# Performance work log

Hardware: AMD Instinct MI355X
Metric: run time of the kernel (lower is better)

Reference implementation:

```python
import jax, jax.numpy as jnp
import numpy as np

B, C, D, O = 64, 64, 512, 256
N_REG, G = 8, 8  # 8 regions of 8 channels


def setup_inputs() -> dict:
    key = jax.random.key(0)
    ks = jax.random.split(key, 9)
    std = 0.02  # init_weights_classify: normal(0, 0.02) for Linear weights, zero bias
    x = jax.random.normal(ks[0], (B, C, D), dtype=jnp.float32)
    region_indices = jnp.arange(C, dtype=jnp.int32).reshape(N_REG, G)
    # attn_fc: Linear(2D -> D), ReLU, Linear(D -> 1)
    W1 = jax.random.normal(ks[1], (2 * D, D), dtype=jnp.float32) * std
    b1 = jnp.zeros((D,), jnp.float32)
    W2 = jax.random.normal(ks[2], (D, 1), dtype=jnp.float32) * std
    b2 = jnp.zeros((1,), jnp.float32)
    # gcn1: Linear(D -> D); gcn2: Linear(D -> O)
    Wg1 = jax.random.normal(ks[3], (D, D), dtype=jnp.float32) * std
    bg1 = jnp.zeros((D,), jnp.float32)
    Wg2 = jax.random.normal(ks[4], (D, O), dtype=jnp.float32) * std
    bg2 = jnp.zeros((O,), jnp.float32)
    return {"x": x, "W1": W1, "b1": b1, "W2": W2, "b2": b2,
            "Wg1": Wg1, "bg1": bg1, "Wg2": Wg2, "bg2": bg2,
            "region_indices": region_indices}


def _leaky_relu02(z):
    return jnp.where(z >= 0, z, 0.2 * z)


def reference(x, W1, b1, W2, b2, Wg1, bg1, Wg2, bg2, region_indices):
    Bb, Cc, Dd = x.shape
    n_reg, g = region_indices.shape
    # channel -> region id; mask[i,j] = same region and i != j
    rid = jnp.zeros((Cc,), jnp.int32).at[region_indices.reshape(-1)].set(
        jnp.repeat(jnp.arange(n_reg, dtype=jnp.int32), g))
    idx = jnp.arange(Cc)
    mask = (rid[:, None] == rid[None, :]) & (idx[:, None] != idx[None, :])  # [C, C]
    # attn_fc on cat(x_i, x_j): split first linear to avoid [B,C,C,2D] concat
    a = x @ W1[:Dd]   # [B, C, D]
    bpart = x @ W1[Dd:]  # [B, C, D]
    h = jax.nn.relu(a[:, :, None, :] + bpart[:, None, :, :] + b1)  # [B, C, C, D]
    scores = jnp.einsum('bijd,do->bij', h, W2) + b2[0]  # [B, C, C]
    scores = jnp.where(mask[None, :, :], scores, -jnp.inf)
    adj = jax.nn.softmax(scores, axis=-1)  # [B, C, C]
    # gcn1: adj @ x -> Linear -> LeakyReLU(0.2); residual mix
    m1 = jnp.einsum('bij,bjd->bid', adj, x)
    x1 = _leaky_relu02(m1 @ Wg1 + bg1)
    x1 = 0.5 * x1 + 0.5 * x
    # gcn2
    m2 = jnp.einsum('bij,bjd->bid', adj, x1)
    out = _leaky_relu02(m2 @ Wg2 + bg2)  # [B, C, O]
    return out
```

## Files before the change

### kernel.cpp

```cpp
#include <hip/hip_runtime.h>
#include <math.h>

typedef __attribute__((ext_vector_type(8))) short s16x8;
typedef __attribute__((ext_vector_type(4))) float f32x4;
typedef unsigned short u16;
typedef unsigned int   u32;

__device__ __forceinline__ float bf2f(u16 u) { return __uint_as_float(((u32)u) << 16); }
__device__ __forceinline__ u16 f2bf(float f) {
    u32 u = __float_as_uint(f);
    return (u16)((u + 0x7FFFu + ((u >> 16) & 1u)) >> 16);
}
__device__ __forceinline__ void gload16(const void* g, void* l) {
    __builtin_amdgcn_global_load_lds((const __attribute__((address_space(1))) u32*)g,
                                     (__attribute__((address_space(3))) u32*)l, 16, 0, 0);
}
__device__ __forceinline__ void xcd_swz(int& bx, int& by) {
    int nx = (int)gridDim.x;
    int L = bx + by * nx;
    int nwg = nx * (int)gridDim.y;
    int nid = (L & 7) * (nwg >> 3) + (L >> 3);
    bx = nid & (nx - 1);
    by = nid / nx;
}

__global__ __launch_bounds__(256)
void prep_kernel(const float* __restrict__ x, u16* __restrict__ x_bf,
                 const float* __restrict__ W1, u16* __restrict__ W1t,
                 const float* __restrict__ Wg1, u16* __restrict__ Wg1t,
                 const float* __restrict__ Wg2, u16* __restrict__ Wg2t)
{
    __shared__ float tile[32][33];
    const int bx = blockIdx.x, tid = threadIdx.x;
    if (bx < 1024) {
        size_t i = ((size_t)bx * 256 + tid) * 8;
        const float4* p = (const float4*)(x + i);
        float4 v0 = p[0], v1 = p[1];
        s16x8 o;
        o[0]=(short)f2bf(v0.x); o[1]=(short)f2bf(v0.y); o[2]=(short)f2bf(v0.z); o[3]=(short)f2bf(v0.w);
        o[4]=(short)f2bf(v1.x); o[5]=(short)f2bf(v1.y); o[6]=(short)f2bf(v1.z); o[7]=(short)f2bf(v1.w);
        *(s16x8*)(x_bf + i) = o;
        return;
    }
    const float* src; u16* dst; int k0, n0, nsrc, obase;
    if (bx < 1536) {
        int idx = bx - 1024, h = idx >> 8, t = idx & 255;
        src = W1 + (size_t)h * 512 * 512; dst = W1t; obase = h * 512;
        k0 = (t >> 4) * 32; n0 = (t & 15) * 32; nsrc = 512;
    } else if (bx < 1792) {
        int t = bx - 1536;
        src = Wg1; dst = Wg1t; obase = 0;
        k0 = (t >> 4) * 32; n0 = (t & 15) * 32; nsrc = 512;
    } else {
        int t = bx - 1792;
        src = Wg2; dst = Wg2t; obase = 0;
        k0 = (t >> 3) * 32; n0 = (t & 7) * 32; nsrc = 256;
    }
    int tx = tid & 31, ty = tid >> 5;
    #pragma unroll
    for (int j = 0; j < 4; j++)
        tile[ty + j * 8][tx] = src[(size_t)(k0 + ty + j * 8) * nsrc + n0 + tx];
    __syncthreads();
    #pragma unroll
    for (int j = 0; j < 4; j++)
        dst[(size_t)(obase + n0 + ty + j * 8) * 512 + k0 + tx] = f2bf(tile[tx][ty + j * 8]);
}

__global__ __launch_bounds__(512)
void gemm1_kernel(const u16* __restrict__ A, const u16* __restrict__ Bt,
                  u16* __restrict__ a_bf, u16* __restrict__ bp_bf)
{
    __shared__ __align__(16) u16 As[2][8192];
    __shared__ __align__(16) u16 Bs[2][8192];

    const int tid = threadIdx.x;
    const int lane = tid & 63, w = tid >> 6;
    const int wr = w >> 1, wc = w & 1;
    const int lr = lane & 15, lq = lane >> 4;
    int bx = blockIdx.x, by = blockIdx.y;
    xcd_swz(bx, by);
    const int m0 = by * 128, n0 = bx * 128;

    const int sr = tid >> 3, ss = tid & 7;
    const int gsl = ss ^ (sr & 7);

    f32x4 acc[2][4] = {};

    auto stage = [&](int buf, int kt) {
        #pragma unroll
        for (int ch = 0; ch < 2; ch++)
            gload16(A + (size_t)(m0 + ch * 64 + sr) * 512 + kt + gsl * 8,
                    &As[buf][ch * 4096 + tid * 8]);
        #pragma unroll
        for (int ch = 0; ch < 2; ch++)
            gload16(Bt + (size_t)(n0 + ch * 64 + sr) * 512 + kt + gsl * 8,
                    &Bs[buf][ch * 4096 + tid * 8]);
    };

    stage(0, 0);
    int cur = 0;
    for (int t = 0; t < 8; t++) {
        __syncthreads();
        if (t < 7) stage(cur ^ 1, (t + 1) * 64);
        const u16* as = As[cur]; const u16* bs = Bs[cur];
        #pragma unroll
        for (int ks = 0; ks < 2; ks++) {
            s16x8 af[2], bfv[4];
            #pragma unroll
            for (int m = 0; m < 2; m++) {
                int r = wr * 32 + m * 16 + lr;
                af[m] = *(const s16x8*)(as + r * 64 + (((ks * 4 + lq) ^ (r & 7)) * 8));
            }
            #pragma unroll
            for (int n = 0; n < 4; n++) {
                int r = wc * 64 + n * 16 + lr;
                bfv[n] = *(const s16x8*)(bs + r * 64 + (((ks * 4 + lq) ^ (r & 7)) * 8));
            }
            #pragma unroll
            for (int m = 0; m < 2; m++)
                #pragma unroll
                for (int n = 0; n < 4; n++)
                    acc[m][n] = __builtin_amdgcn_mfma_f32_16x16x32_bf16(af[m], bfv[n], acc[m][n], 0, 0, 0);
        }
        cur ^= 1;
    }

    #pragma unroll
    for (int m = 0; m < 2; m++)
        #pragma unroll
        for (int n = 0; n < 4; n++)
            #pragma unroll
            for (int j = 0; j < 4; j++) {
                int row = m0 + wr * 32 + m * 16 + lq * 4 + j;
                int col = n0 + wc * 64 + n * 16 + lr;
                u16 v = f2bf(acc[m][n][j]);
                if (col < 512) a_bf [(size_t)row * 512 + col] = v;
                else           bp_bf[(size_t)row * 512 + col - 512] = v;
            }
}

__global__ __launch_bounds__(256)
void scores_kernel(const u16* __restrict__ a_bf, const u16* __restrict__ bp_bf,
                   const u16* __restrict__ x_bf,
                   const float* __restrict__ b1, const float* __restrict__ W2,
                   const float* __restrict__ b2,
                   const int* __restrict__ region_indices,
                   float* __restrict__ adjw, u16* __restrict__ m1_bf)
{
    __shared__ __align__(16) u16 bpL[16 * 512];
    __shared__ __align__(16) u16 xL[16 * 512];
    __shared__ int memS[16];

    int L = blockIdx.x;
    int nid = ((L & 7) << 5) + (L >> 3);
    const int b = nid >> 2, q = nid & 3;
    const int tid = threadIdx.x, lane = tid & 63, w = tid >> 6;

    if (tid < 16) memS[tid] = region_indices[q * 16 + tid];
    __syncthreads();

    #pragma unroll
    for (int it = 0; it < 4; it++) {
        int rl = it * 4 + w;
        size_t src = (size_t)(b * 64 + memS[rl]) * 512 + lane * 8;
        gload16(bp_bf + src, bpL + rl * 512 + lane * 8);
        gload16(x_bf  + src, xL  + rl * 512 + lane * 8);
    }

    const int d0 = lane * 8;
    float4 b1a = *(const float4*)(b1 + d0), b1b = *(const float4*)(b1 + d0 + 4);
    float4 w2a = *(const float4*)(W2 + d0), w2b = *(const float4*)(W2 + d0 + 4);
    float b1v[8] = { b1a.x, b1a.y, b1a.z, b1a.w, b1b.x, b1b.y, b1b.z, b1b.w };
    float w2v[8] = { w2a.x, w2a.y, w2a.z, w2a.w, w2b.x, w2b.y, w2b.z, w2b.w };
    const float bias2 = b2[0];
    __syncthreads();

    for (int rr = 0; rr < 4; rr++) {
        const int rl = w * 4 + rr;
        const int rhalf = rl >> 3, s_slot = rl & 7;
        const int i = memS[rl];
        const int bi = b * 64 + i;

        s16x8 a8 = *(const s16x8*)(a_bf + (size_t)bi * 512 + d0);
        float ai[8];
        #pragma unroll
        for (int t = 0; t < 8; t++) ai[t] = bf2f((u16)a8[t]) + b1v[t];

        float p[8];
        #pragma unroll
        for (int m = 0; m < 8; m++) {
            s16x8 bv = *(const s16x8*)(bpL + (rhalf * 8 + m) * 512 + d0);
            float s = 0.f;
            #pragma unroll
            for (int t = 0; t < 8; t++) {
                float h = ai[t] + bf2f((u16)bv[t]);
                s += fmaxf(h, 0.f) * w2v[t];
            }
            p[m] = s;
        }
        #pragma unroll
        for (int off = 32; off >= 1; off >>= 1)
            #pragma unroll
            for (int m = 0; m < 8; m++) p[m] += __shfl_xor(p[m], off);

        float scmax = -INFINITY;
        #pragma unroll
        for (int m = 0; m < 8; m++) {
            p[m] = (m == s_slot) ? -INFINITY : p[m] + bias2;
            scmax = fmaxf(scmax, p[m]);
        }
        float esum = 0.f;
        #pragma unroll
        for (int m = 0; m < 8; m++) {
            p[m] = (m == s_slot) ? 0.f : __expf(p[m] - scmax);
            esum += p[m];
        }
        const float inv = 1.f / esum;

        float accv[8] = {};
        #pragma unroll
        for (int m = 0; m < 8; m++) {
            p[m] *= inv;
            s16x8 xv = *(const s16x8*)(xL + (rhalf * 8 + m) * 512 + d0);
            #pragma unroll
            for (int t = 0; t < 8; t++) accv[t] += p[m] * bf2f((u16)xv[t]);
        }
        s16x8 o;
        #pragma unroll
        for (int t = 0; t < 8; t++) o[t] = (short)f2bf(accv[t]);
        *(s16x8*)(m1_bf + (size_t)bi * 512 + d0) = o;
        if (lane < 8) adjw[(size_t)bi * 8 + lane] = p[lane];
    }
}

__global__ __launch_bounds__(512)
void gemm2_m2_kernel(const u16* __restrict__ A, const u16* __restrict__ Bt,
                     const float* __restrict__ bias,
                     const float* __restrict__ adjw, const int* __restrict__ region_indices,
                     u16* __restrict__ m2)
{
    __shared__ __align__(16) u16 As[2][4096];
    __shared__ __align__(16) u16 Bs[2][8192];
    __shared__ __align__(16) u16 y1s[64 * 136];
    __shared__ int ri[64], rid[64];

    const int tid = threadIdx.x;
    const int lane = tid & 63, w = tid >> 6;
    const int wr = w >> 2, wc = w & 3;
    const int lr = lane & 15, lq = lane >> 4;
    int bx = blockIdx.x, by = blockIdx.y;
    xcd_swz(bx, by);
    const int b = by, n0 = bx * 128, m0 = b * 64;

    const int sr = tid >> 3, ss = tid & 7, gsl = ss ^ (sr & 7);

    if (tid < 64) { int c = region_indices[tid]; ri[tid] = c; rid[c] = tid >> 3; }

    f32x4 acc[2][2] = {};

    auto stage = [&](int buf, int kt) {
        gload16(A + (size_t)(m0 + sr) * 512 + kt + gsl * 8, &As[buf][tid * 8]);
        #pragma unroll
        for (int ch = 0; ch < 2; ch++)
            gload16(Bt + (size_t)(n0 + ch * 64 + sr) * 512 + kt + gsl * 8,
                    &Bs[buf][ch * 4096 + tid * 8]);
    };

    stage(0, 0);
    int cur = 0;
    for (int t = 0; t < 8; t++) {
        __syncthreads();
        if (t < 7) stage(cur ^ 1, (t + 1) * 64);
        const u16* as = As[cur]; const u16* bs = Bs[cur];
        #pragma unroll
        for (int ks = 0; ks < 2; ks++) {
            s16x8 af[2], bfv[2];
            #pragma unroll
            for (int m = 0; m < 2; m++) {
                int r = wr * 32 + m * 16 + lr;
                af[m] = *(const s16x8*)(as + r * 64 + (((ks * 4 + lq) ^ (r & 7)) * 8));
            }
            #pragma unroll
            for (int n = 0; n < 2; n++) {
                int r = wc * 32 + n * 16 + lr;
                bfv[n] = *(const s16x8*)(bs + r * 64 + (((ks * 4 + lq) ^ (r & 7)) * 8));
            }
            #pragma unroll
            for (int m = 0; m < 2; m++)
                #pragma unroll
                for (int n = 0; n < 2; n++)
                    acc[m][n] = __builtin_amdgcn_mfma_f32_16x16x32_bf16(af[m], bfv[n], acc[m][n], 0, 0, 0);
        }
        cur ^= 1;
    }

    #pragma unroll
    for (int m = 0; m < 2; m++)
        #pragma unroll
        for (int n = 0; n < 2; n++)
            #pragma unroll
            for (int j = 0; j < 4; j++) {
                int lrow = wr * 32 + m * 16 + lq * 4 + j;
                int lcol = wc * 32 + n * 16 + lr;
                float v = acc[m][n][j] + bias[n0 + lcol];
                v = (v >= 0.f) ? v : 0.2f * v;
                y1s[lrow * 136 + lcol] = f2bf(v);
            }
    __syncthreads();

    const int i = tid >> 3, cb = tid & 7, c0 = cb * 16;
    const int bi = m0 + i;
    const int r = rid[i];
    float acc2[16] = {};
    #pragma unroll
    for (int m = 0; m < 8; m++) {
        float wm = adjw[(size_t)bi * 8 + m];
        int j = ri[r * 8 + m];
        #pragma unroll
        for (int cc = 0; cc < 2; cc++) {
            s16x8 v = *(const s16x8*)(y1s + j * 136 + c0 + cc * 8);
            #pragma unroll
            for (int t = 0; t < 8; t++) acc2[cc * 8 + t] += wm * bf2f((u16)v[t]);
        }
    }
    #pragma unroll
    for (int cc = 0; cc < 2; cc++) {
        s16x8 m1v = *(const s16x8*)(A + (size_t)bi * 512 + n0 + c0 + cc * 8);
        s16x8 o;
        #pragma unroll
        for (int t = 0; t < 8; t++)
            o[t] = (short)f2bf(0.5f * acc2[cc * 8 + t] + 0.5f * bf2f((u16)m1v[t]));
        *(s16x8*)(m2 + (size_t)bi * 512 + n0 + c0 + cc * 8) = o;
    }
}

__global__ __launch_bounds__(256)
void gemm3_kernel(const u16* __restrict__ A, const u16* __restrict__ Bt,
                  const float* __restrict__ bias, float* __restrict__ Of)
{
    __shared__ __align__(16) u16 As[2][4096];
    __shared__ __align__(16) u16 Bs[2][4096];

    const int tid = threadIdx.x;
    const int lane = tid & 63, w = tid >> 6;
    const int wr = w >> 1, wc = w & 1;
    const int lr = lane & 15, lq = lane >> 4;
    int bx = blockIdx.x, by = blockIdx.y;
    xcd_swz(bx, by);
    const int m0 = by * 64, n0 = bx * 64;

    const int sr = tid >> 3, ss = tid & 7, gsl = ss ^ (sr & 7);

    f32x4 acc[2][2] = {};

    auto stage = [&](int buf, int kt) {
        #pragma unroll
        for (int ch = 0; ch < 2; ch++)
            gload16(A + (size_t)(m0 + ch * 32 + sr) * 512 + kt + gsl * 8,
                    &As[buf][ch * 2048 + tid * 8]);
        #pragma unroll
        for (int ch = 0; ch < 2; ch++)
            gload16(Bt + (size_t)(n0 + ch * 32 + sr) * 512 + kt + gsl * 8,
                    &Bs[buf][ch * 2048 + tid * 8]);
    };

    stage(0, 0);
    int cur = 0;
    for (int t = 0; t < 8; t++) {
        __syncthreads();
        if (t < 7) stage(cur ^ 1, (t + 1) * 64);
        const u16* as = As[cur]; const u16* bs = Bs[cur];
        #pragma unroll
        for (int ks = 0; ks < 2; ks++) {
            s16x8 af[2], bfv[2];
            #pragma unroll
            for (int m = 0; m < 2; m++) {
                int r = wr * 32 + m * 16 + lr;
                af[m] = *(const s16x8*)(as + r * 64 + (((ks * 4 + lq) ^ (r & 7)) * 8));
            }
            #pragma unroll
            for (int n = 0; n < 2; n++) {
                int r = wc * 32 + n * 16 + lr;
                bfv[n] = *(const s16x8*)(bs + r * 64 + (((ks * 4 + lq) ^ (r & 7)) * 8));
            }
            #pragma unroll
            for (int m = 0; m < 2; m++)
                #pragma unroll
                for (int n = 0; n < 2; n++)
                    acc[m][n] = __builtin_amdgcn_mfma_f32_16x16x32_bf16(af[m], bfv[n], acc[m][n], 0, 0, 0);
        }
        cur ^= 1;
    }

    #pragma unroll
    for (int m = 0; m < 2; m++)
        #pragma unroll
        for (int n = 0; n < 2; n++)
            #pragma unroll
            for (int j = 0; j < 4; j++) {
                int row = m0 + wr * 32 + m * 16 + lq * 4 + j;
                int col = n0 + wc * 32 + n * 16 + lr;
                float v = acc[m][n][j] + bias[col];
                v = (v >= 0.f) ? v : 0.2f * v;
                Of[(size_t)row * 256 + col] = v;
            }
}

extern "C" void kernel_launch(void* const* d_in, const int* in_sizes, int n_in,
                              void* d_out, int out_size, void* d_ws, size_t ws_size,
                              hipStream_t stream) {
    const float* x    = (const float*)d_in[0];
    const float* W1   = (const float*)d_in[1];
    const float* b1   = (const float*)d_in[2];
    const float* W2   = (const float*)d_in[3];
    const float* b2   = (const float*)d_in[4];
    const float* Wg1  = (const float*)d_in[5];
    const float* bg1  = (const float*)d_in[6];
    const float* Wg2  = (const float*)d_in[7];
    const float* bg2  = (const float*)d_in[8];
    const int* region_indices = (const int*)d_in[9];
    float* out = (float*)d_out;

    char* ws = (char*)d_ws;
    const size_t MB = 1024 * 1024;
    u16* x_bf  = (u16*)(ws);
    u16* W1t   = (u16*)(ws + 4 * MB);
    u16* Wg1t  = (u16*)(ws + 5 * MB);
    u16* Wg2t  = (u16*)(ws + 5 * MB + 512 * 1024);
    u16* a_bf  = (u16*)(ws + 6 * MB);
    u16* bp_bf = (u16*)(ws + 10 * MB);
    u16* m1_bf = (u16*)(ws + 14 * MB);
    u16* m2_bf = (u16*)(ws + 18 * MB);
    float* adjw = (float*)(ws + 22 * MB);

    prep_kernel<<<1920, 256, 0, stream>>>(x, x_bf, W1, W1t, Wg1, Wg1t, Wg2, Wg2t);

    gemm1_kernel<<<dim3(8, 32), 512, 0, stream>>>(x_bf, W1t, a_bf, bp_bf);

    scores_kernel<<<256, 256, 0, stream>>>(a_bf, bp_bf, x_bf, b1, W2, b2,
                                           region_indices, adjw, m1_bf);

    gemm2_m2_kernel<<<dim3(4, 64), 512, 0, stream>>>(
        m1_bf, Wg1t, bg1, adjw, region_indices, m2_bf);

    gemm3_kernel<<<dim3(4, 64), 256, 0, stream>>>(m2_bf, Wg2t, bg2, out);
}
```

Before: 118.2 us.

## Reassociate gcn1 as adj@(x@Wg1) and fuse region stages into one kernel

Uses linearity, adj@(x)@Wg1 = adj@(x@Wg1), to fold the Wg1 projection into the first GEMM as extra output columns (N grows from 1024 to 1536). A single per-(batch,region) kernel then computes the scores, the softmax, both adjacency mixes, the bias, the LeakyReLU and the residual entirely in LDS. This removes the separate scores and gemm2 kernels, one launch, and the round trips of adjw and m1 through memory. The trade-off is a wider first GEMM, small 64-thread blocks in the region kernel, and a different bf16 rounding point.

```diff
diff --git a/kernel.cpp b/kernel.cpp
--- a/kernel.cpp
+++ b/kernel.cpp
@@ -26,9 +26,9 @@
 
 __global__ __launch_bounds__(256)
 void prep_kernel(const float* __restrict__ x, u16* __restrict__ x_bf,
-                 const float* __restrict__ W1, u16* __restrict__ W1t,
-                 const float* __restrict__ Wg1, u16* __restrict__ Wg1t,
-                 const float* __restrict__ Wg2, u16* __restrict__ Wg2t)
+                 const float* __restrict__ W1, u16* __restrict__ Bt,
+                 const float* __restrict__ Wg1, const float* __restrict__ Wg2,
+                 u16* __restrict__ Wg2t)
 {
     __shared__ float tile[32][33];
     const int bx = blockIdx.x, tid = threadIdx.x;
@@ -45,11 +45,11 @@
     const float* src; u16* dst; int k0, n0, nsrc, obase;
     if (bx < 1536) {
         int idx = bx - 1024, h = idx >> 8, t = idx & 255;
-        src = W1 + (size_t)h * 512 * 512; dst = W1t; obase = h * 512;
+        src = W1 + (size_t)h * 512 * 512; dst = Bt; obase = h * 512;
         k0 = (t >> 4) * 32; n0 = (t & 15) * 32; nsrc = 512;
     } else if (bx < 1792) {
         int t = bx - 1536;
-        src = Wg1; dst = Wg1t; obase = 0;
+        src = Wg1; dst = Bt; obase = 1024;
         k0 = (t >> 4) * 32; n0 = (t & 15) * 32; nsrc = 512;
     } else {
         int t = bx - 1792;
@@ -68,7 +68,7 @@
 
 __global__ __launch_bounds__(512)
 void gemm1_kernel(const u16* __restrict__ A, const u16* __restrict__ Bt,
-                  u16* __restrict__ a_bf, u16* __restrict__ bp_bf)
+                  u16* __restrict__ a_bf, u16* __restrict__ bp_bf, u16* __restrict__ v_bf)
 {
     __shared__ __align__(16) u16 As[2][8192];
     __shared__ __align__(16) u16 Bs[2][8192];
@@ -77,8 +77,10 @@
     const int lane = tid & 63, w = tid >> 6;
     const int wr = w >> 1, wc = w & 1;
     const int lr = lane & 15, lq = lane >> 4;
-    int bx = blockIdx.x, by = blockIdx.y;
-    xcd_swz(bx, by);
+
+    int L = blockIdx.y * 12 + blockIdx.x;
+    int nid = (L & 7) * 48 + (L >> 3);
+    const int by = nid / 12, bx = nid - by * 12;
     const int m0 = by * 128, n0 = bx * 128;
 
     const int sr = tid >> 3, ss = tid & 7;
@@ -134,203 +136,144 @@
                 int row = m0 + wr * 32 + m * 16 + lq * 4 + j;
                 int col = n0 + wc * 64 + n * 16 + lr;
                 u16 v = f2bf(acc[m][n][j]);
-                if (col < 512) a_bf [(size_t)row * 512 + col] = v;
-                else           bp_bf[(size_t)row * 512 + col - 512] = v;
-            }
-}
-
-__global__ __launch_bounds__(256)
-void scores_kernel(const u16* __restrict__ a_bf, const u16* __restrict__ bp_bf,
-                   const u16* __restrict__ x_bf,
+                if (col < 512)       a_bf [(size_t)row * 512 + col] = v;
+                else if (col < 1024) bp_bf[(size_t)row * 512 + col - 512] = v;
+                else                 v_bf [(size_t)row * 512 + col - 1024] = v;
+            }
+}
+
+__global__ __launch_bounds__(64)
+void region_kernel(const u16* __restrict__ a_bf, const u16* __restrict__ bp_bf,
+                   const u16* __restrict__ x_bf, const u16* __restrict__ v_bf,
                    const float* __restrict__ b1, const float* __restrict__ W2,
-                   const float* __restrict__ b2,
-                   const int* __restrict__ region_indices,
-                   float* __restrict__ adjw, u16* __restrict__ m1_bf)
+                   const float* __restrict__ b2, const float* __restrict__ bg1,
+                   const int* __restrict__ region_indices, u16* __restrict__ m2_bf)
 {
-    __shared__ __align__(16) u16 bpL[16 * 512];
-    __shared__ __align__(16) u16 xL[16 * 512];
-    __shared__ int memS[16];
-
-    int L = blockIdx.x;
-    int nid = ((L & 7) << 5) + (L >> 3);
-    const int b = nid >> 2, q = nid & 3;
-    const int tid = threadIdx.x, lane = tid & 63, w = tid >> 6;
-
-    if (tid < 16) memS[tid] = region_indices[q * 16 + tid];
-    __syncthreads();
-
-    #pragma unroll
-    for (int it = 0; it < 4; it++) {
-        int rl = it * 4 + w;
-        size_t src = (size_t)(b * 64 + memS[rl]) * 512 + lane * 8;
-        gload16(bp_bf + src, bpL + rl * 512 + lane * 8);
-        gload16(x_bf  + src, xL  + rl * 512 + lane * 8);
-    }
-
+    __shared__ __align__(16) u16 aL[8 * 512];
+    __shared__ __align__(16) u16 bpL[8 * 512];
+    __shared__ __align__(16) u16 xL[8 * 512];
+    __shared__ __align__(16) u16 vL[8 * 512];
+    __shared__ float adjS[8][8];
+
+    const int blk = blockIdx.x;
+    const int b = blk >> 3, r = blk & 7;
+    const int lane = threadIdx.x;
     const int d0 = lane * 8;
-    float4 b1a = *(const float4*)(b1 + d0), b1b = *(const float4*)(b1 + d0 + 4);
-    float4 w2a = *(const float4*)(W2 + d0), w2b = *(const float4*)(W2 + d0 + 4);
+
+    int mem[8];
+    #pragma unroll
+    for (int j = 0; j < 8; j++) mem[j] = region_indices[r * 8 + j];
+
+    #pragma unroll
+    for (int j = 0; j < 8; j++) {
+        size_t src = (size_t)(b * 64 + mem[j]) * 512 + d0;
+        gload16(a_bf  + src, aL  + j * 512 + d0);
+        gload16(bp_bf + src, bpL + j * 512 + d0);
+        gload16(x_bf  + src, xL  + j * 512 + d0);
+        gload16(v_bf  + src, vL  + j * 512 + d0);
+    }
+    float4 b1a = *(const float4*)(b1 + d0),  b1b = *(const float4*)(b1 + d0 + 4);
+    float4 w2a = *(const float4*)(W2 + d0),  w2b = *(const float4*)(W2 + d0 + 4);
+    float4 g1a = *(const float4*)(bg1 + d0), g1b = *(const float4*)(bg1 + d0 + 4);
     float b1v[8] = { b1a.x, b1a.y, b1a.z, b1a.w, b1b.x, b1b.y, b1b.z, b1b.w };
     float w2v[8] = { w2a.x, w2a.y, w2a.z, w2a.w, w2b.x, w2b.y, w2b.z, w2b.w };
+    float bgv[8] = { g1a.x, g1a.y, g1a.z, g1a.w, g1b.x, g1b.y, g1b.z, g1b.w };
     const float bias2 = b2[0];
     __syncthreads();
 
-    for (int rr = 0; rr < 4; rr++) {
-        const int rl = w * 4 + rr;
-        const int rhalf = rl >> 3, s_slot = rl & 7;
-        const int i = memS[rl];
-        const int bi = b * 64 + i;
-
-        s16x8 a8 = *(const s16x8*)(a_bf + (size_t)bi * 512 + d0);
+    #pragma unroll
+    for (int i = 0; i < 8; i++) {
+        s16x8 av = *(const s16x8*)(aL + i * 512 + d0);
         float ai[8];
         #pragma unroll
-        for (int t = 0; t < 8; t++) ai[t] = bf2f((u16)a8[t]) + b1v[t];
+        for (int t = 0; t < 8; t++) ai[t] = bf2f((u16)av[t]) + b1v[t];
 
         float p[8];
         #pragma unroll
-        for (int m = 0; m < 8; m++) {
-            s16x8 bv = *(const s16x8*)(bpL + (rhalf * 8 + m) * 512 + d0);
+        for (int j = 0; j < 8; j++) {
+            s16x8 bv = *(const s16x8*)(bpL + j * 512 + d0);
             float s = 0.f;
             #pragma unroll
             for (int t = 0; t < 8; t++) {
                 float h = ai[t] + bf2f((u16)bv[t]);
                 s += fmaxf(h, 0.f) * w2v[t];
             }
-            p[m] = s;
+            p[j] = s;
         }
         #pragma unroll
         for (int off = 32; off >= 1; off >>= 1)
             #pragma unroll
-            for (int m = 0; m < 8; m++) p[m] += __shfl_xor(p[m], off);
+            for (int j = 0; j < 8; j++) p[j] += __shfl_xor(p[j], off);
 
         float scmax = -INFINITY;
         #pragma unroll
-        for (int m = 0; m < 8; m++) {
-            p[m] = (m == s_slot) ? -INFINITY : p[m] + bias2;
-            scmax = fmaxf(scmax, p[m]);
+        for (int j = 0; j < 8; j++) {
+            p[j] = (j == i) ? -INFINITY : p[j] + bias2;
+            scmax = fmaxf(scmax, p[j]);
         }
         float esum = 0.f;
         #pragma unroll
-        for (int m = 0; m < 8; m++) {
-            p[m] = (m == s_slot) ? 0.f : __expf(p[m] - scmax);
-            esum += p[m];
+        for (int j = 0; j < 8; j++) {
+            p[j] = (j == i) ? 0.f : __expf(p[j] - scmax);
+            esum += p[j];
         }
         const float inv = 1.f / esum;
 
         float accv[8] = {};
         #pragma unroll
-        for (int m = 0; m < 8; m++) {
-            p[m] *= inv;
-            s16x8 xv = *(const s16x8*)(xL + (rhalf * 8 + m) * 512 + d0);
-            #pragma unroll
-            for (int t = 0; t < 8; t++) accv[t] += p[m] * bf2f((u16)xv[t]);
+        for (int j = 0; j < 8; j++) {
+            p[j] *= inv;
+            s16x8 xv = *(const s16x8*)(xL + j * 512 + d0);
+            #pragma unroll
+            for (int t = 0; t < 8; t++) accv[t] += p[j] * bf2f((u16)xv[t]);
         }
         s16x8 o;
         #pragma unroll
         for (int t = 0; t < 8; t++) o[t] = (short)f2bf(accv[t]);
-        *(s16x8*)(m1_bf + (size_t)bi * 512 + d0) = o;
-        if (lane < 8) adjw[(size_t)bi * 8 + lane] = p[lane];
-    }
-}
-
-__global__ __launch_bounds__(512)
-void gemm2_m2_kernel(const u16* __restrict__ A, const u16* __restrict__ Bt,
-                     const float* __restrict__ bias,
-                     const float* __restrict__ adjw, const int* __restrict__ region_indices,
-                     u16* __restrict__ m2)
-{
-    __shared__ __align__(16) u16 As[2][4096];
-    __shared__ __align__(16) u16 Bs[2][8192];
-    __shared__ __align__(16) u16 y1s[64 * 136];
-    __shared__ int ri[64], rid[64];
-
-    const int tid = threadIdx.x;
-    const int lane = tid & 63, w = tid >> 6;
-    const int wr = w >> 2, wc = w & 3;
-    const int lr = lane & 15, lq = lane >> 4;
-    int bx = blockIdx.x, by = blockIdx.y;
-    xcd_swz(bx, by);
-    const int b = by, n0 = bx * 128, m0 = b * 64;
-
-    const int sr = tid >> 3, ss = tid & 7, gsl = ss ^ (sr & 7);
-
-    if (tid < 64) { int c = region_indices[tid]; ri[tid] = c; rid[c] = tid >> 3; }
-
-    f32x4 acc[2][2] = {};
-
-    auto stage = [&](int buf, int kt) {
-        gload16(A + (size_t)(m0 + sr) * 512 + kt + gsl * 8, &As[buf][tid * 8]);
-        #pragma unroll
-        for (int ch = 0; ch < 2; ch++)
-            gload16(Bt + (size_t)(n0 + ch * 64 + sr) * 512 + kt + gsl * 8,
-                    &Bs[buf][ch * 4096 + tid * 8]);
-    };
-
-    stage(0, 0);
-    int cur = 0;
-    for (int t = 0; t < 8; t++) {
-        __syncthreads();
-        if (t < 7) stage(cur ^ 1, (t + 1) * 64);
-        const u16* as = As[cur]; const u16* bs = Bs[cur];
-        #pragma unroll
-        for (int ks = 0; ks < 2; ks++) {
-            s16x8 af[2], bfv[2];
-            #pragma unroll
-            for (int m = 0; m < 2; m++) {
-                int r = wr * 32 + m * 16 + lr;
-                af[m] = *(const s16x8*)(as + r * 64 + (((ks * 4 + lq) ^ (r & 7)) * 8));
-            }
-            #pragma unroll
-            for (int n = 0; n < 2; n++) {
-                int r = wc * 32 + n * 16 + lr;
-                bfv[n] = *(const s16x8*)(bs + r * 64 + (((ks * 4 + lq) ^ (r & 7)) * 8));
-            }
-            #pragma unroll
-            for (int m = 0; m < 2; m++)
-                #pragma unroll
-                for (int n = 0; n < 2; n++)
-                    acc[m][n] = __builtin_amdgcn_mfma_f32_16x16x32_bf16(af[m], bfv[n], acc[m][n], 0, 0, 0);
-        }
-        cur ^= 1;
-    }
-
-    #pragma unroll
-    for (int m = 0; m < 2; m++)
-        #pragma unroll
-        for (int n = 0; n < 2; n++)
-            #pragma unroll
-            for (int j = 0; j < 4; j++) {
-                int lrow = wr * 32 + m * 16 + lq * 4 + j;
-                int lcol = wc * 32 + n * 16 + lr;
-                float v = acc[m][n][j] + bias[n0 + lcol];
-                v = (v >= 0.f) ? v : 0.2f * v;
-                y1s[lrow * 136 + lcol] = f2bf(v);
-            }
+        *(s16x8*)(aL + i * 512 + d0) = o;
+        if (lane < 8) adjS[i][lane] = p[lane];
+    }
     __syncthreads();
 
-    const int i = tid >> 3, cb = tid & 7, c0 = cb * 16;
-    const int bi = m0 + i;
-    const int r = rid[i];
-    float acc2[16] = {};
-    #pragma unroll
-    for (int m = 0; m < 8; m++) {
-        float wm = adjw[(size_t)bi * 8 + m];
-        int j = ri[r * 8 + m];
-        #pragma unroll
-        for (int cc = 0; cc < 2; cc++) {
-            s16x8 v = *(const s16x8*)(y1s + j * 136 + c0 + cc * 8);
-            #pragma unroll
-            for (int t = 0; t < 8; t++) acc2[cc * 8 + t] += wm * bf2f((u16)v[t]);
-        }
-    }
-    #pragma unroll
-    for (int cc = 0; cc < 2; cc++) {
-        s16x8 m1v = *(const s16x8*)(A + (size_t)bi * 512 + n0 + c0 + cc * 8);
+    #pragma unroll
+    for (int j = 0; j < 8; j++) {
+        float acc[8];
+        #pragma unroll
+        for (int t = 0; t < 8; t++) acc[t] = bgv[t];
+        #pragma unroll
+        for (int k = 0; k < 8; k++) {
+            float wk = adjS[j][k];
+            s16x8 vv = *(const s16x8*)(vL + k * 512 + d0);
+            #pragma unroll
+            for (int t = 0; t < 8; t++) acc[t] += wk * bf2f((u16)vv[t]);
+        }
         s16x8 o;
         #pragma unroll
+        for (int t = 0; t < 8; t++) {
+            float v = acc[t];
+            v = (v >= 0.f) ? v : 0.2f * v;
+            o[t] = (short)f2bf(v);
+        }
+        *(s16x8*)(bpL + j * 512 + d0) = o;
+    }
+    __syncthreads();
+
+    #pragma unroll
+    for (int i = 0; i < 8; i++) {
+        float acc[8] = {};
+        #pragma unroll
+        for (int j = 0; j < 8; j++) {
+            float wj = adjS[i][j];
+            s16x8 yv = *(const s16x8*)(bpL + j * 512 + d0);
+            #pragma unroll
+            for (int t = 0; t < 8; t++) acc[t] += wj * bf2f((u16)yv[t]);
+        }
+        s16x8 m1v = *(const s16x8*)(aL + i * 512 + d0);
+        s16x8 o;
+        #pragma unroll
         for (int t = 0; t < 8; t++)
-            o[t] = (short)f2bf(0.5f * acc2[cc * 8 + t] + 0.5f * bf2f((u16)m1v[t]));
-        *(s16x8*)(m2 + (size_t)bi * 512 + n0 + c0 + cc * 8) = o;
+            o[t] = (short)f2bf(0.5f * acc[t] + 0.5f * bf2f((u16)m1v[t]));
+        *(s16x8*)(m2_bf + (size_t)(b * 64 + mem[i]) * 512 + d0) = o;
     }
 }
 
@@ -424,24 +367,19 @@
     char* ws = (char*)d_ws;
     const size_t MB = 1024 * 1024;
     u16* x_bf  = (u16*)(ws);
-    u16* W1t   = (u16*)(ws + 4 * MB);
-    u16* Wg1t  = (u16*)(ws + 5 * MB);
-    u16* Wg2t  = (u16*)(ws + 5 * MB + 512 * 1024);
-    u16* a_bf  = (u16*)(ws + 6 * MB);
-    u16* bp_bf = (u16*)(ws + 10 * MB);
-    u16* m1_bf = (u16*)(ws + 14 * MB);
-    u16* m2_bf = (u16*)(ws + 18 * MB);
-    float* adjw = (float*)(ws + 22 * MB);
-
-    prep_kernel<<<1920, 256, 0, stream>>>(x, x_bf, W1, W1t, Wg1, Wg1t, Wg2, Wg2t);
-
-    gemm1_kernel<<<dim3(8, 32), 512, 0, stream>>>(x_bf, W1t, a_bf, bp_bf);
-
-    scores_kernel<<<256, 256, 0, stream>>>(a_bf, bp_bf, x_bf, b1, W2, b2,
-                                           region_indices, adjw, m1_bf);
-
-    gemm2_m2_kernel<<<dim3(4, 64), 512, 0, stream>>>(
-        m1_bf, Wg1t, bg1, adjw, region_indices, m2_bf);
+    u16* Bt    = (u16*)(ws + 4 * MB);
+    u16* Wg2t  = (u16*)(ws + 6 * MB);
+    u16* a_bf  = (u16*)(ws + 8 * MB);
+    u16* bp_bf = (u16*)(ws + 12 * MB);
+    u16* v_bf  = (u16*)(ws + 16 * MB);
+    u16* m2_bf = (u16*)(ws + 20 * MB);
+
+    prep_kernel<<<1920, 256, 0, stream>>>(x, x_bf, W1, Bt, Wg1, Wg2, Wg2t);
+
+    gemm1_kernel<<<dim3(12, 32), 512, 0, stream>>>(x_bf, Bt, a_bf, bp_bf, v_bf);
+
+    region_kernel<<<512, 64, 0, stream>>>(a_bf, bp_bf, x_bf, v_bf, b1, W2, b2,
+                                          bg1, region_indices, m2_bf);
 
     gemm3_kernel<<<dim3(4, 64), 256, 0, stream>>>(m2_bf, Wg2t, bg2, out);
 }
```

After: 121.6 us. 2.9% more time.

## Fuse attention scores, m1 aggregation and gcn1 GEMM into one kernel

Applied to the files above, without the earlier changes.

Merges the scores/softmax/aggregation kernel with the gcn1 GEMM kernel so each block keeps a whole batch's m1 in LDS (swizzled) and feeds it straight to MFMA, along with the adjacency weights. This removes a kernel launch and the global write and read of m1 and adjw. In exchange, each of the four column-tile blocks per batch recomputes the full score and aggregation work, quadrupling that work. The large LDS footprint also limits occupancy to one block per CU.

```diff
diff --git a/kernel.cpp b/kernel.cpp
--- a/kernel.cpp
+++ b/kernel.cpp
@@ -139,33 +139,33 @@
             }
 }
 
-__global__ __launch_bounds__(256)
-void scores_kernel(const u16* __restrict__ a_bf, const u16* __restrict__ bp_bf,
-                   const u16* __restrict__ x_bf,
-                   const float* __restrict__ b1, const float* __restrict__ W2,
-                   const float* __restrict__ b2,
-                   const int* __restrict__ region_indices,
-                   float* __restrict__ adjw, u16* __restrict__ m1_bf)
+__global__ __launch_bounds__(512)
+void mid_kernel(const u16* __restrict__ a_bf, const u16* __restrict__ bp_bf,
+                const u16* __restrict__ x_bf,
+                const float* __restrict__ b1, const float* __restrict__ W2,
+                const float* __restrict__ b2,
+                const u16* __restrict__ Wg1t, const float* __restrict__ bg1,
+                const int* __restrict__ region_indices, u16* __restrict__ m2_bf)
 {
-    __shared__ __align__(16) u16 bpL[16 * 512];
-    __shared__ __align__(16) u16 xL[16 * 512];
-    __shared__ int memS[16];
+    __shared__ __align__(16) u16 bpm1[64 * 512];
+    __shared__ __align__(16) u16 xbuf[64 * 512];
+    __shared__ float adjS[64][8];
+    __shared__ int ri[64], rid[64];
+
+    const int tid = threadIdx.x, lane = tid & 63, w = tid >> 6;
+    const int lr = lane & 15, lq = lane >> 4;
+    const int sr = tid >> 3, gsl = (tid & 7) ^ (sr & 7);
 
     int L = blockIdx.x;
     int nid = ((L & 7) << 5) + (L >> 3);
-    const int b = nid >> 2, q = nid & 3;
-    const int tid = threadIdx.x, lane = tid & 63, w = tid >> 6;
-
-    if (tid < 16) memS[tid] = region_indices[q * 16 + tid];
-    __syncthreads();
-
-    #pragma unroll
-    for (int it = 0; it < 4; it++) {
-        int rl = it * 4 + w;
-        size_t src = (size_t)(b * 64 + memS[rl]) * 512 + lane * 8;
-        gload16(bp_bf + src, bpL + rl * 512 + lane * 8);
-        gload16(x_bf  + src, xL  + rl * 512 + lane * 8);
-    }
+    const int b = nid >> 2, n0 = (nid & 3) * 128;
+
+    #pragma unroll
+    for (int it = 0; it < 8; it++) {
+        gload16(bp_bf + (size_t)b * 32768 + it * 4096 + tid * 8, bpm1 + it * 4096 + tid * 8);
+        gload16(x_bf  + (size_t)b * 32768 + it * 4096 + tid * 8, xbuf + it * 4096 + tid * 8);
+    }
+    if (tid < 64) { int c = region_indices[tid]; ri[tid] = c; rid[c] = tid >> 3; }
 
     const int d0 = lane * 8;
     float4 b1a = *(const float4*)(b1 + d0), b1b = *(const float4*)(b1 + d0 + 4);
@@ -175,13 +175,14 @@
     const float bias2 = b2[0];
     __syncthreads();
 
-    for (int rr = 0; rr < 4; rr++) {
-        const int rl = w * 4 + rr;
-        const int rhalf = rl >> 3, s_slot = rl & 7;
-        const int i = memS[rl];
-        const int bi = b * 64 + i;
-
-        s16x8 a8 = *(const s16x8*)(a_bf + (size_t)bi * 512 + d0);
+    int mem[8];
+    #pragma unroll
+    for (int j = 0; j < 8; j++) mem[j] = ri[w * 8 + j];
+
+    #pragma unroll
+    for (int j = 0; j < 8; j++) {
+        const int i = mem[j];
+        s16x8 a8 = *(const s16x8*)(a_bf + (size_t)(b * 64 + i) * 512 + d0);
         float ai[8];
         #pragma unroll
         for (int t = 0; t < 8; t++) ai[t] = bf2f((u16)a8[t]) + b1v[t];
@@ -189,7 +190,7 @@
         float p[8];
         #pragma unroll
         for (int m = 0; m < 8; m++) {
-            s16x8 bv = *(const s16x8*)(bpL + (rhalf * 8 + m) * 512 + d0);
+            s16x8 bv = *(const s16x8*)(bpm1 + mem[m] * 512 + d0);
             float s = 0.f;
             #pragma unroll
             for (int t = 0; t < 8; t++) {
@@ -206,84 +207,69 @@
         float scmax = -INFINITY;
         #pragma unroll
         for (int m = 0; m < 8; m++) {
-            p[m] = (m == s_slot) ? -INFINITY : p[m] + bias2;
+            p[m] = (m == j) ? -INFINITY : p[m] + bias2;
             scmax = fmaxf(scmax, p[m]);
         }
         float esum = 0.f;
         #pragma unroll
         for (int m = 0; m < 8; m++) {
-            p[m] = (m == s_slot) ? 0.f : __expf(p[m] - scmax);
+            p[m] = (m == j) ? 0.f : __expf(p[m] - scmax);
             esum += p[m];
         }
         const float inv = 1.f / esum;
-
+        if (lane < 8) adjS[i][lane] = p[lane] * inv;
+    }
+
+    #pragma unroll
+    for (int j = 0; j < 8; j++) {
+        const int i = mem[j];
+        float wv[8];
+        #pragma unroll
+        for (int m = 0; m < 8; m++) wv[m] = adjS[i][m];
         float accv[8] = {};
         #pragma unroll
         for (int m = 0; m < 8; m++) {
-            p[m] *= inv;
-            s16x8 xv = *(const s16x8*)(xL + (rhalf * 8 + m) * 512 + d0);
-            #pragma unroll
-            for (int t = 0; t < 8; t++) accv[t] += p[m] * bf2f((u16)xv[t]);
+            s16x8 xv = *(const s16x8*)(xbuf + mem[m] * 512 + d0);
+            #pragma unroll
+            for (int t = 0; t < 8; t++) accv[t] += wv[m] * bf2f((u16)xv[t]);
         }
         s16x8 o;
         #pragma unroll
         for (int t = 0; t < 8; t++) o[t] = (short)f2bf(accv[t]);
-        *(s16x8*)(m1_bf + (size_t)bi * 512 + d0) = o;
-        if (lane < 8) adjw[(size_t)bi * 8 + lane] = p[lane];
-    }
-}
-
-__global__ __launch_bounds__(512)
-void gemm2_m2_kernel(const u16* __restrict__ A, const u16* __restrict__ Bt,
-                     const float* __restrict__ bias,
-                     const float* __restrict__ adjw, const int* __restrict__ region_indices,
-                     u16* __restrict__ m2)
-{
-    __shared__ __align__(16) u16 As[2][4096];
-    __shared__ __align__(16) u16 Bs[2][8192];
-    __shared__ __align__(16) u16 y1s[64 * 136];
-    __shared__ int ri[64], rid[64];
-
-    const int tid = threadIdx.x;
-    const int lane = tid & 63, w = tid >> 6;
+        *(s16x8*)(bpm1 + i * 512 + ((lane ^ (i & 7)) * 8)) = o;
+    }
+    __syncthreads();
+
+    u16* Bsm = xbuf;
+    u16* y1s = xbuf + 16384;
     const int wr = w >> 2, wc = w & 3;
-    const int lr = lane & 15, lq = lane >> 4;
-    int bx = blockIdx.x, by = blockIdx.y;
-    xcd_swz(bx, by);
-    const int b = by, n0 = bx * 128, m0 = b * 64;
-
-    const int sr = tid >> 3, ss = tid & 7, gsl = ss ^ (sr & 7);
-
-    if (tid < 64) { int c = region_indices[tid]; ri[tid] = c; rid[c] = tid >> 3; }
-
     f32x4 acc[2][2] = {};
 
-    auto stage = [&](int buf, int kt) {
-        gload16(A + (size_t)(m0 + sr) * 512 + kt + gsl * 8, &As[buf][tid * 8]);
+    auto stageB = [&](int buf, int kt) {
         #pragma unroll
         for (int ch = 0; ch < 2; ch++)
-            gload16(Bt + (size_t)(n0 + ch * 64 + sr) * 512 + kt + gsl * 8,
-                    &Bs[buf][ch * 4096 + tid * 8]);
+            gload16(Wg1t + (size_t)(n0 + ch * 64 + sr) * 512 + kt + gsl * 8,
+                    Bsm + buf * 8192 + ch * 4096 + tid * 8);
     };
-
-    stage(0, 0);
+    stageB(0, 0);
     int cur = 0;
     for (int t = 0; t < 8; t++) {
         __syncthreads();
-        if (t < 7) stage(cur ^ 1, (t + 1) * 64);
-        const u16* as = As[cur]; const u16* bs = Bs[cur];
+        if (t < 7) stageB(cur ^ 1, (t + 1) * 64);
+        const u16* bs = Bsm + cur * 8192;
         #pragma unroll
         for (int ks = 0; ks < 2; ks++) {
             s16x8 af[2], bfv[2];
             #pragma unroll
             for (int m = 0; m < 2; m++) {
                 int r = wr * 32 + m * 16 + lr;
-                af[m] = *(const s16x8*)(as + r * 64 + (((ks * 4 + lq) ^ (r & 7)) * 8));
+                int slot = t * 8 + ks * 4 + lq;
+                af[m] = *(const s16x8*)(bpm1 + r * 512 + ((slot ^ (r & 7)) * 8));
             }
             #pragma unroll
             for (int n = 0; n < 2; n++) {
-                int r = wc * 32 + n * 16 + lr;
-                bfv[n] = *(const s16x8*)(bs + r * 64 + (((ks * 4 + lq) ^ (r & 7)) * 8));
+                int rb = wc * 32 + n * 16 + lr;
+                bfv[n] = *(const s16x8*)(bs + rb * 64 + (((ks * 4 + lq) ^ (rb & 7)) * 8));
             }
             #pragma unroll
             for (int m = 0; m < 2; m++)
@@ -293,7 +279,6 @@
         }
         cur ^= 1;
     }
-
     #pragma unroll
     for (int m = 0; m < 2; m++)
         #pragma unroll
@@ -302,19 +287,18 @@
             for (int j = 0; j < 4; j++) {
                 int lrow = wr * 32 + m * 16 + lq * 4 + j;
                 int lcol = wc * 32 + n * 16 + lr;
-                float v = acc[m][n][j] + bias[n0 + lcol];
+                float v = acc[m][n][j] + bg1[n0 + lcol];
                 v = (v >= 0.f) ? v : 0.2f * v;
                 y1s[lrow * 136 + lcol] = f2bf(v);
             }
     __syncthreads();
 
     const int i = tid >> 3, cb = tid & 7, c0 = cb * 16;
-    const int bi = m0 + i;
     const int r = rid[i];
     float acc2[16] = {};
     #pragma unroll
     for (int m = 0; m < 8; m++) {
-        float wm = adjw[(size_t)bi * 8 + m];
+        float wm = adjS[i][m];
         int j = ri[r * 8 + m];
         #pragma unroll
         for (int cc = 0; cc < 2; cc++) {
@@ -325,12 +309,13 @@
     }
     #pragma unroll
     for (int cc = 0; cc < 2; cc++) {
-        s16x8 m1v = *(const s16x8*)(A + (size_t)bi * 512 + n0 + c0 + cc * 8);
+        int slot = (n0 + c0) / 8 + cc;
+        s16x8 m1v = *(const s16x8*)(bpm1 + i * 512 + ((slot ^ (i & 7)) * 8));
         s16x8 o;
         #pragma unroll
         for (int t = 0; t < 8; t++)
             o[t] = (short)f2bf(0.5f * acc2[cc * 8 + t] + 0.5f * bf2f((u16)m1v[t]));
-        *(s16x8*)(m2 + (size_t)bi * 512 + n0 + c0 + cc * 8) = o;
+        *(s16x8*)(m2_bf + (size_t)(b * 64 + i) * 512 + n0 + c0 + cc * 8) = o;
     }
 }
 
@@ -429,19 +414,14 @@
     u16* Wg2t  = (u16*)(ws + 5 * MB + 512 * 1024);
     u16* a_bf  = (u16*)(ws + 6 * MB);
     u16* bp_bf = (u16*)(ws + 10 * MB);
-    u16* m1_bf = (u16*)(ws + 14 * MB);
-    u16* m2_bf = (u16*)(ws + 18 * MB);
-    float* adjw = (float*)(ws + 22 * MB);
+    u16* m2_bf = (u16*)(ws + 14 * MB);
 
     prep_kernel<<<1920, 256, 0, stream>>>(x, x_bf, W1, W1t, Wg1, Wg1t, Wg2, Wg2t);
 
     gemm1_kernel<<<dim3(8, 32), 512, 0, stream>>>(x_bf, W1t, a_bf, bp_bf);
 
-    scores_kernel<<<256, 256, 0, stream>>>(a_bf, bp_bf, x_bf, b1, W2, b2,
-                                           region_indices, adjw, m1_bf);
-
-    gemm2_m2_kernel<<<dim3(4, 64), 512, 0, stream>>>(
-        m1_bf, Wg1t, bg1, adjw, region_indices, m2_bf);
+    mid_kernel<<<256, 512, 0, stream>>>(a_bf, bp_bf, x_bf, b1, W2, b2,
+                                        Wg1t, bg1, region_indices, m2_bf);
 
     gemm3_kernel<<<dim3(4, 64), 256, 0, stream>>>(m2_bf, Wg2t, bg2, out);
 }
```

New measurement: 122.8 us. 3.8% more time.
